# Optimization experiments

Hardware: AMD Instinct MI355X
Metric: run time of the kernel (lower is better)

## Reference

```python
import math
import jax, jax.numpy as jnp
import numpy as np

MAX_RADIUS = 10.0
N_BASIS = 10   # number_of_basis
H = 100        # radial MLP hidden width
EPS = 1e-6


def _radial(r, w1, w2, w3):
    """CosineBasisModel: cosine-bump radial basis followed by a swish MLP.
    r: [B,N,N] pair distances -> [B,N,N,C*C] per-pair kernel weights."""
    radii = jnp.linspace(0.0, MAX_RADIUS, N_BASIS)
    step = radii[1] - radii[0]
    u = (r[..., None] - radii) / step * (jnp.pi / 2)            # [B,N,N,R]
    basis = jnp.where(jnp.abs(u) < jnp.pi / 2, jnp.cos(u) ** 2, 0.0)
    h1 = jax.nn.silu(basis @ w1 * (1.0 / math.sqrt(N_BASIS)))  # swish, fan-in norm (e3nn FC)
    h2 = jax.nn.silu(h1 @ w2 * (1.0 / math.sqrt(H)))
    return h2 @ w3 * (1.0 / math.sqrt(H))                       # [B,N,N,C*C]


def setup_inputs() -> dict:
    key = jax.random.key(0)
    ks = jax.random.split(key, 10)
    B, N1, N2, C = 8, 32, 32, 64
    return {
        "input1": jax.random.normal(ks[0], (B, N1, C), jnp.float32),
        "input2": jax.random.normal(ks[1], (B, N2, C), jnp.float32),
        "xyz1": jax.random.normal(ks[2], (B, N1, 3), jnp.float32) * 3.0,
        "xyz2": jax.random.normal(ks[3], (B, N2, 3), jnp.float32) * 3.0,
        "mask": jnp.ones((B, N1 + N2), jnp.int32),
        "w1": jax.random.normal(ks[4], (N_BASIS, H), jnp.float32),
        "w2": jax.random.normal(ks[5], (H, H), jnp.float32),
        "w3": jax.random.normal(ks[6], (H, C * C), jnp.float32),
        "fc3_w": jax.random.normal(ks[7], (C, C), jnp.float32),
        "fc2_w": jax.random.normal(ks[8], (C, 1), jnp.float32),
    }


def reference(input1, input2, xyz1, xyz2, mask, w1, w2, w3, fc3_w, fc2_w):
    x = jnp.concatenate((input1, input2), axis=1)        # [B,N,C]
    xyz = jnp.concatenate((xyz1, xyz2), axis=1)          # [B,N,3]
    B, N, C = x.shape
    # continuous-filter convolution: per-pair radial kernel, all-pairs scatter-sum
    diff = xyz[:, :, None, :] - xyz[:, None, :, :]       # [B,N,N,3]
    r = jnp.sqrt(jnp.sum(diff * diff, axis=-1) + 1e-12)  # [B,N,N]
    K = _radial(r, w1, w2, w3).reshape(B, N, N, C, C)    # [B,N,N,Cout,Cin]
    x = jnp.einsum('zaboi,zbi->zao', K, x) * (1.0 / math.sqrt(N))
    # Norm over irreps: for l=0 scalar irreps the norm is |x|
    x = jnp.abs(x)
    x = jnp.where(mask[:, :, None] != 0, x, 0.0)
    x = jnp.sum(x, axis=1)                               # [B,C]
    mean = x.mean(-1, keepdims=True)
    std = jnp.std(x, axis=-1, ddof=1, keepdims=True)     # torch.std is unbiased
    x = (x - mean) / (std + EPS)
    x = jax.nn.leaky_relu(x @ fc3_w * (1.0 / math.sqrt(C)))
    x = x @ fc2_w * (1.0 / math.sqrt(C))
    return jax.nn.sigmoid(x).reshape(-1)                 # [B]
```

## Files before the change

kernel.cpp:

```cpp
#include <hip/hip_runtime.h>
#include <math.h>

#define NB 10
#define HH 100
#define TABN 2048
#define TAB_MAX 11.2f
#define INV_DELTA ((float)TABN / TAB_MAX)


__global__ __launch_bounds__(256) void tm_kernel(
    const float* __restrict__ in1, const float* __restrict__ in2,
    const float* __restrict__ w1, const float* __restrict__ w2,
    const float* __restrict__ w3,
    float* __restrict__ tab, float* __restrict__ Mout)
{
    __shared__ float s_w1[NB * HH];
    __shared__ float s_basis[8][NB];
    __shared__ float s_h1[8][HH];
    __shared__ float s_x[16][64];

    int tid = threadIdx.x;

    if (blockIdx.x < 257) {
        for (int i = tid; i < NB * HH; i += 256) s_w1[i] = w1[i];

        int p0 = blockIdx.x * 8;
        const float DELTA = TAB_MAX / (float)TABN;
        const float STEP = 10.0f / 9.0f;
        const float HALF_PI = 1.57079632679489662f;

        if (tid < 8 * NB) {
            int p = tid / NB, j = tid % NB;
            float r = (float)(p0 + p) * DELTA;
            float u = (r - (float)j * STEP) * (HALF_PI / STEP);
            float c = __cosf(u);
            s_basis[p][j] = (fabsf(u) < HALF_PI) ? c * c : 0.0f;
        }
        __syncthreads();

        const float inv_sqrt10 = 0.31622776601683794f;
        for (int task = tid; task < 8 * HH; task += 256) {
            int p = task / HH, k = task % HH;
            float acc = 0.f;
            #pragma unroll
            for (int j = 0; j < NB; ++j) acc += s_basis[p][j] * s_w1[j * HH + k];
            acc *= inv_sqrt10;
            float sg = 1.0f / (1.0f + __expf(-acc));
            s_h1[p][k] = acc * sg;
        }
        __syncthreads();

        if (tid < 8 * 25) {
            int p = tid / 25, k2g = tid % 25;
            int idx = p0 + p;
            float4 acc = make_float4(0.f, 0.f, 0.f, 0.f);
            #pragma unroll 4
            for (int k = 0; k < HH; ++k) {
                float hv = s_h1[p][k];
                float4 wv = *(const float4*)(w2 + (size_t)k * HH + k2g * 4);
                acc.x += hv * wv.x; acc.y += hv * wv.y; acc.z += hv * wv.z; acc.w += hv * wv.w;
            }
            if (idx <= TABN) {
                float4 o; float a;
                a = acc.x * 0.1f; o.x = a / (1.0f + __expf(-a));
                a = acc.y * 0.1f; o.y = a / (1.0f + __expf(-a));
                a = acc.z * 0.1f; o.z = a / (1.0f + __expf(-a));
                a = acc.w * 0.1f; o.w = a / (1.0f + __expf(-a));
                *(float4*)(tab + (size_t)idx * HH + k2g * 4) = o;
            }
        }
    } else {
        int m = blockIdx.x - 257;
        int zbg = m / 7, yc = m % 7;

        {
            int lz = tid >> 4, q = tid & 15;
            int zb = zbg * 16 + lz;
            int z = zb >> 6, b = zb & 63;
            const float* src = (b < 32) ? (in1 + (size_t)(z * 32 + b) * 64)
                                        : (in2 + (size_t)(z * 32 + (b - 32)) * 64);
            *(float4*)&s_x[lz][q * 4] = *(const float4*)(src + q * 4);
        }
        __syncthreads();

        int task = yc * 256 + tid;
        if (task < 1600) {
            int h = task >> 4, og = task & 15;
            const float* wbase = w3 + (size_t)h * 4096 + og * 4 * 64;

            float4 acc[16];
            #pragma unroll
            for (int l = 0; l < 16; ++l) acc[l] = make_float4(0.f, 0.f, 0.f, 0.f);

            const float4* sx4 = (const float4*)s_x;
            #pragma unroll 2
            for (int i4 = 0; i4 < 16; ++i4) {
                float4 wa = *(const float4*)(wbase + 0 * 64 + i4 * 4);
                float4 wb = *(const float4*)(wbase + 1 * 64 + i4 * 4);
                float4 wc = *(const float4*)(wbase + 2 * 64 + i4 * 4);
                float4 wd = *(const float4*)(wbase + 3 * 64 + i4 * 4);
                #pragma unroll
                for (int l = 0; l < 16; ++l) {
                    float4 xv = sx4[l * 16 + i4];
                    acc[l].x += wa.x * xv.x + wa.y * xv.y + wa.z * xv.z + wa.w * xv.w;
                    acc[l].y += wb.x * xv.x + wb.y * xv.y + wb.z * xv.z + wb.w * xv.w;
                    acc[l].z += wc.x * xv.x + wc.y * xv.y + wc.z * xv.z + wc.w * xv.w;
                    acc[l].w += wd.x * xv.x + wd.y * xv.y + wd.z * xv.z + wd.w * xv.w;
                }
            }
            #pragma unroll
            for (int l = 0; l < 16; ++l) {
                int zb = zbg * 16 + l;
                *(float4*)(Mout + (size_t)zb * 6400 + h * 64 + og * 4) = acc[l];
            }
        }
    }
}

__global__ __launch_bounds__(256) void kernel_Y(
    const float* __restrict__ xyz1, const float* __restrict__ xyz2,
    const float* __restrict__ tab, const float* __restrict__ M,
    float* __restrict__ partial)
{
    __shared__ float s_M[100 * 64];
    __shared__ float s_h2T[100 * 64];
    __shared__ int   s_i0[64];
    __shared__ float s_f[64];

    int z = blockIdx.x, b = blockIdx.y;
    int tid = threadIdx.x;

    if (tid < 64) {
        int a = tid;
        const float* pa = (a < 32) ? (xyz1 + (size_t)(z * 32 + a) * 3)
                                   : (xyz2 + (size_t)(z * 32 + (a - 32)) * 3);
        const float* pb = (b < 32) ? (xyz1 + (size_t)(z * 32 + b) * 3)
                                   : (xyz2 + (size_t)(z * 32 + (b - 32)) * 3);
        float dx = pa[0] - pb[0], dy = pa[1] - pb[1], dz = pa[2] - pb[2];
        float r = sqrtf(dx * dx + dy * dy + dz * dz + 1e-12f);
        float t = r * INV_DELTA;
        int i0 = (int)t;
        i0 = (i0 < TABN - 1) ? i0 : (TABN - 1);
        float f = t - (float)i0;
        s_i0[a] = i0;
        s_f[a] = (f < 1.0f) ? f : 1.0f;
    }

    {
        const float4* Msrc = (const float4*)(M + (size_t)(z * 64 + b) * 6400);
        float4* sM4 = (float4*)s_M;
        for (int i = tid; i < 1600; i += 256) sM4[i] = Msrc[i];
    }
    __syncthreads();

    for (int task = tid; task < 1600; task += 256) {
        int a4 = task / 100, c = task - a4 * 100;
        float4 hv;
        #pragma unroll
        for (int k = 0; k < 4; ++k) {
            int a = a4 * 4 + k;
            int i0 = s_i0[a];
            float f = s_f[a];
            float v0 = tab[(size_t)i0 * HH + c];
            float v1 = tab[(size_t)i0 * HH + HH + c];
            ((float*)&hv)[k] = fmaf(f, v1 - v0, v0);
        }
        *(float4*)&s_h2T[c * 64 + ((a4 ^ (c & 7)) << 2)] = hv;
    }
    __syncthreads();

    int og = tid & 15, ag = tid >> 4;
    float4 acc0 = make_float4(0.f, 0.f, 0.f, 0.f);
    float4 acc1 = make_float4(0.f, 0.f, 0.f, 0.f);
    float4 acc2 = make_float4(0.f, 0.f, 0.f, 0.f);
    float4 acc3 = make_float4(0.f, 0.f, 0.f, 0.f);

    #pragma unroll 4
    for (int c = 0; c < 100; ++c) {
        float4 mv = *(const float4*)&s_M[c * 64 + og * 4];
        float4 hv = *(const float4*)&s_h2T[c * 64 + ((ag ^ (c & 7)) << 2)];
        acc0.x += hv.x * mv.x; acc0.y += hv.x * mv.y; acc0.z += hv.x * mv.z; acc0.w += hv.x * mv.w;
        acc1.x += hv.y * mv.x; acc1.y += hv.y * mv.y; acc1.z += hv.y * mv.z; acc1.w += hv.y * mv.w;
        acc2.x += hv.z * mv.x; acc2.y += hv.z * mv.y; acc2.z += hv.z * mv.z; acc2.w += hv.z * mv.w;
        acc3.x += hv.w * mv.x; acc3.y += hv.w * mv.y; acc3.z += hv.w * mv.z; acc3.w += hv.w * mv.w;
    }

    size_t base = ((size_t)(b * 8 + z) * 64 + ag * 4) * 64 + og * 4;
    *(float4*)&partial[base]       = acc0;
    *(float4*)&partial[base + 64]  = acc1;
    *(float4*)&partial[base + 128] = acc2;
    *(float4*)&partial[base + 192] = acc3;
}

__global__ __launch_bounds__(256) void kernel_red(
    const float* __restrict__ partial, const int* __restrict__ mask,
    float* __restrict__ s2)
{
    __shared__ float sred[4][64];
    int z = blockIdx.x, ac = blockIdx.y;
    int tid = threadIdx.x;
    int o = tid & 63, ar = tid >> 6;
    int a = ac * 4 + ar;

    float val = 0.f;
    #pragma unroll 8
    for (int b = 0; b < 64; ++b)
        val += partial[((size_t)(b * 8 + z) * 64 + a) * 64 + o];

    const float scale = 0.0125f;
    float m = (mask[z * 64 + a] != 0) ? 1.0f : 0.0f;
    sred[ar][o] = fabsf(val) * scale * m;
    __syncthreads();

    if (tid < 64)
        s2[((size_t)z * 16 + ac) * 64 + o] = sred[0][o] + sred[1][o] + sred[2][o] + sred[3][o];
}

__global__ __launch_bounds__(64) void kernel_final(
    const float* __restrict__ s2, const float* __restrict__ fc3w,
    const float* __restrict__ fc2w, float* __restrict__ out)
{
    __shared__ float s_sn[64];
    int z = blockIdx.x;
    int o = threadIdx.x;

    float s = 0.f;
    #pragma unroll
    for (int ac = 0; ac < 16; ++ac)
        s += s2[((size_t)z * 16 + ac) * 64 + o];

    float tot = s;
    #pragma unroll
    for (int d = 32; d >= 1; d >>= 1) tot += __shfl_xor(tot, d, 64);
    float mean = tot * (1.0f / 64.0f);
    float dv = s - mean;
    float v2 = dv * dv;
    #pragma unroll
    for (int d = 32; d >= 1; d >>= 1) v2 += __shfl_xor(v2, d, 64);
    float var = v2 * (1.0f / 63.0f);
    float sn = dv / (sqrtf(var) + 1e-6f);

    s_sn[o] = sn;
    __syncthreads();

    float acc = 0.f;
    #pragma unroll 8
    for (int i = 0; i < 64; ++i) acc += s_sn[i] * fc3w[i * 64 + o];
    acc *= 0.125f;
    float t = (acc > 0.f) ? acc : 0.01f * acc;

    float pr = t * fc2w[o];
    #pragma unroll
    for (int d = 32; d >= 1; d >>= 1) pr += __shfl_xor(pr, d, 64);
    if (o == 0) out[z] = 1.0f / (1.0f + expf(-0.125f * pr));
}

extern "C" void kernel_launch(void* const* d_in, const int* in_sizes, int n_in,
                              void* d_out, int out_size, void* d_ws, size_t ws_size,
                              hipStream_t stream) {
    const float* in1  = (const float*)d_in[0];
    const float* in2  = (const float*)d_in[1];
    const float* xyz1 = (const float*)d_in[2];
    const float* xyz2 = (const float*)d_in[3];
    const int*   mask = (const int*)d_in[4];
    const float* w1   = (const float*)d_in[5];
    const float* w2   = (const float*)d_in[6];
    const float* w3   = (const float*)d_in[7];
    const float* fc3w = (const float*)d_in[8];
    const float* fc2w = (const float*)d_in[9];
    float* out = (float*)d_out;

    float* ws      = (float*)d_ws;
    float* tab     = ws;
    float* M       = ws + 204900;
    float* partial = ws + 3481700;
    float* s2      = ws + 5578852;

    tm_kernel<<<481, 256, 0, stream>>>(in1, in2, w1, w2, w3, tab, M);
    kernel_Y<<<dim3(8, 64), 256, 0, stream>>>(xyz1, xyz2, tab, M, partial);
    kernel_red<<<dim3(8, 16), 256, 0, stream>>>(partial, mask, s2);
    kernel_final<<<8, 64, 0, stream>>>(s2, fc3w, fc2w, out);
}
```

Measured before the change: 54.87 us.

## Fuse reduction and final MLP, halve kernel_Y threads, read x directly

Merges the reduction and final-MLP kernels into one kernel, launching one 256-thread block per batch element. Each thread now sums partials across all b with float4 loads before the normalisation and MLP. kernel_Y drops to 128 threads, each computing 8 output rows instead of 4, and the partial layout changes to z-major. The M-precompute path in tm_kernel reads x straight from global memory instead of staging it in LDS. Fewer launches and less LDS traffic come at the cost of far fewer blocks in the final reduction and more register pressure in kernel_Y.

```diff
diff --git a/kernel.cpp b/kernel.cpp
--- a/kernel.cpp
+++ b/kernel.cpp
@@ -17,7 +17,6 @@
     __shared__ float s_w1[NB * HH];
     __shared__ float s_basis[8][NB];
     __shared__ float s_h1[8][HH];
-    __shared__ float s_x[16][64];
 
     int tid = threadIdx.x;
 
@@ -73,35 +72,31 @@
         int m = blockIdx.x - 257;
         int zbg = m / 7, yc = m % 7;
 
-        {
-            int lz = tid >> 4, q = tid & 15;
-            int zb = zbg * 16 + lz;
-            int z = zb >> 6, b = zb & 63;
-            const float* src = (b < 32) ? (in1 + (size_t)(z * 32 + b) * 64)
-                                        : (in2 + (size_t)(z * 32 + (b - 32)) * 64);
-            *(float4*)&s_x[lz][q * 4] = *(const float4*)(src + q * 4);
-        }
-        __syncthreads();
-
+        const float* xp[16];
+        #pragma unroll
+        for (int l = 0; l < 16; ++l) {
+            int zb = zbg * 16 + l, z = zb >> 6, b = zb & 63;
+            xp[l] = (b < 32) ? (in1 + (size_t)(z * 32 + b) * 64)
+                             : (in2 + (size_t)(z * 32 + (b - 32)) * 64);
+        }
         int task = yc * 256 + tid;
         if (task < 1600) {
             int h = task >> 4, og = task & 15;
-            const float* wbase = w3 + (size_t)h * 4096 + og * 4 * 64;
+            const float* wbase = w3 + (size_t)h * 4096 + og * 256;
 
             float4 acc[16];
             #pragma unroll
             for (int l = 0; l < 16; ++l) acc[l] = make_float4(0.f, 0.f, 0.f, 0.f);
 
-            const float4* sx4 = (const float4*)s_x;
             #pragma unroll 2
             for (int i4 = 0; i4 < 16; ++i4) {
-                float4 wa = *(const float4*)(wbase + 0 * 64 + i4 * 4);
-                float4 wb = *(const float4*)(wbase + 1 * 64 + i4 * 4);
-                float4 wc = *(const float4*)(wbase + 2 * 64 + i4 * 4);
-                float4 wd = *(const float4*)(wbase + 3 * 64 + i4 * 4);
+                float4 wa = *(const float4*)(wbase + i4 * 4);
+                float4 wb = *(const float4*)(wbase + 64 + i4 * 4);
+                float4 wc = *(const float4*)(wbase + 128 + i4 * 4);
+                float4 wd = *(const float4*)(wbase + 192 + i4 * 4);
                 #pragma unroll
                 for (int l = 0; l < 16; ++l) {
-                    float4 xv = sx4[l * 16 + i4];
+                    float4 xv = *(const float4*)(xp[l] + i4 * 4);
                     acc[l].x += wa.x * xv.x + wa.y * xv.y + wa.z * xv.z + wa.w * xv.w;
                     acc[l].y += wb.x * xv.x + wb.y * xv.y + wb.z * xv.z + wb.w * xv.w;
                     acc[l].z += wc.x * xv.x + wc.y * xv.y + wc.z * xv.z + wc.w * xv.w;
@@ -117,18 +112,18 @@
     }
 }
 
-__global__ __launch_bounds__(256) void kernel_Y(
+__global__ __launch_bounds__(128) void kernel_Y(
     const float* __restrict__ xyz1, const float* __restrict__ xyz2,
     const float* __restrict__ tab, const float* __restrict__ M,
     float* __restrict__ partial)
 {
-    __shared__ float s_M[100 * 64];
-    __shared__ float s_h2T[100 * 64];
+    __shared__ float s_M[6400];
+    __shared__ float s_h2T[6400];
     __shared__ int   s_i0[64];
     __shared__ float s_f[64];
 
-    int z = blockIdx.x, b = blockIdx.y;
-    int tid = threadIdx.x;
+    const int b = blockIdx.x, z = blockIdx.y;
+    const int tid = threadIdx.x;
 
     if (tid < 64) {
         int a = tid;
@@ -145,114 +140,132 @@
         s_i0[a] = i0;
         s_f[a] = (f < 1.0f) ? f : 1.0f;
     }
-
     {
         const float4* Msrc = (const float4*)(M + (size_t)(z * 64 + b) * 6400);
         float4* sM4 = (float4*)s_M;
-        for (int i = tid; i < 1600; i += 256) sM4[i] = Msrc[i];
-    }
-    __syncthreads();
-
-    for (int task = tid; task < 1600; task += 256) {
-        int a4 = task / 100, c = task - a4 * 100;
-        float4 hv;
+        for (int i = tid; i < 1600; i += 128) sM4[i] = Msrc[i];
+    }
+    __syncthreads();
+
+    {
+        int a4 = tid >> 3;
+        int cg2 = tid & 7;
+        int i0a[4]; float fa[4];
         #pragma unroll
         for (int k = 0; k < 4; ++k) {
-            int a = a4 * 4 + k;
-            int i0 = s_i0[a];
-            float f = s_f[a];
-            float v0 = tab[(size_t)i0 * HH + c];
-            float v1 = tab[(size_t)i0 * HH + HH + c];
-            ((float*)&hv)[k] = fmaf(f, v1 - v0, v0);
-        }
-        *(float4*)&s_h2T[c * 64 + ((a4 ^ (c & 7)) << 2)] = hv;
-    }
-    __syncthreads();
-
-    int og = tid & 15, ag = tid >> 4;
-    float4 acc0 = make_float4(0.f, 0.f, 0.f, 0.f);
-    float4 acc1 = make_float4(0.f, 0.f, 0.f, 0.f);
-    float4 acc2 = make_float4(0.f, 0.f, 0.f, 0.f);
-    float4 acc3 = make_float4(0.f, 0.f, 0.f, 0.f);
+            i0a[k] = s_i0[a4 * 4 + k];
+            fa[k]  = s_f[a4 * 4 + k];
+        }
+        for (int c = cg2; c < 100; c += 8) {
+            float4 hv;
+            #pragma unroll
+            for (int k = 0; k < 4; ++k) {
+                const float* tp = tab + (size_t)i0a[k] * HH + c;
+                float v0 = tp[0], v1 = tp[HH];
+                ((float*)&hv)[k] = fmaf(fa[k], v1 - v0, v0);
+            }
+            *(float4*)&s_h2T[c * 64 + ((a4 ^ (c & 7)) << 2)] = hv;
+        }
+    }
+    __syncthreads();
+
+    const int og = tid & 15;
+    const int ag = tid >> 4;
+    float4 acc[8];
+    #pragma unroll
+    for (int k = 0; k < 8; ++k) acc[k] = make_float4(0.f, 0.f, 0.f, 0.f);
 
     #pragma unroll 4
     for (int c = 0; c < 100; ++c) {
+        float4 hv0 = *(const float4*)&s_h2T[c * 64 + (((2 * ag) ^ (c & 7)) << 2)];
+        float4 hv1 = *(const float4*)&s_h2T[c * 64 + (((2 * ag + 1) ^ (c & 7)) << 2)];
         float4 mv = *(const float4*)&s_M[c * 64 + og * 4];
-        float4 hv = *(const float4*)&s_h2T[c * 64 + ((ag ^ (c & 7)) << 2)];
-        acc0.x += hv.x * mv.x; acc0.y += hv.x * mv.y; acc0.z += hv.x * mv.z; acc0.w += hv.x * mv.w;
-        acc1.x += hv.y * mv.x; acc1.y += hv.y * mv.y; acc1.z += hv.y * mv.z; acc1.w += hv.y * mv.w;
-        acc2.x += hv.z * mv.x; acc2.y += hv.z * mv.y; acc2.z += hv.z * mv.z; acc2.w += hv.z * mv.w;
-        acc3.x += hv.w * mv.x; acc3.y += hv.w * mv.y; acc3.z += hv.w * mv.z; acc3.w += hv.w * mv.w;
-    }
-
-    size_t base = ((size_t)(b * 8 + z) * 64 + ag * 4) * 64 + og * 4;
-    *(float4*)&partial[base]       = acc0;
-    *(float4*)&partial[base + 64]  = acc1;
-    *(float4*)&partial[base + 128] = acc2;
-    *(float4*)&partial[base + 192] = acc3;
-}
-
-__global__ __launch_bounds__(256) void kernel_red(
+        acc[0].x += hv0.x * mv.x; acc[0].y += hv0.x * mv.y; acc[0].z += hv0.x * mv.z; acc[0].w += hv0.x * mv.w;
+        acc[1].x += hv0.y * mv.x; acc[1].y += hv0.y * mv.y; acc[1].z += hv0.y * mv.z; acc[1].w += hv0.y * mv.w;
+        acc[2].x += hv0.z * mv.x; acc[2].y += hv0.z * mv.y; acc[2].z += hv0.z * mv.z; acc[2].w += hv0.z * mv.w;
+        acc[3].x += hv0.w * mv.x; acc[3].y += hv0.w * mv.y; acc[3].z += hv0.w * mv.z; acc[3].w += hv0.w * mv.w;
+        acc[4].x += hv1.x * mv.x; acc[4].y += hv1.x * mv.y; acc[4].z += hv1.x * mv.z; acc[4].w += hv1.x * mv.w;
+        acc[5].x += hv1.y * mv.x; acc[5].y += hv1.y * mv.y; acc[5].z += hv1.y * mv.z; acc[5].w += hv1.y * mv.w;
+        acc[6].x += hv1.z * mv.x; acc[6].y += hv1.z * mv.y; acc[6].z += hv1.z * mv.z; acc[6].w += hv1.z * mv.w;
+        acc[7].x += hv1.w * mv.x; acc[7].y += hv1.w * mv.y; acc[7].z += hv1.w * mv.z; acc[7].w += hv1.w * mv.w;
+    }
+
+    size_t base = ((size_t)(z * 64 + b) * 64 + ag * 8) * 64 + og * 4;
+    #pragma unroll
+    for (int k = 0; k < 8; ++k)
+        *(float4*)&partial[base + (size_t)k * 64] = acc[k];
+}
+
+__global__ __launch_bounds__(256) void kernel_rf(
     const float* __restrict__ partial, const int* __restrict__ mask,
-    float* __restrict__ s2)
+    const float* __restrict__ fc3w, const float* __restrict__ fc2w,
+    float* __restrict__ out)
 {
-    __shared__ float sred[4][64];
-    int z = blockIdx.x, ac = blockIdx.y;
-    int tid = threadIdx.x;
-    int o = tid & 63, ar = tid >> 6;
-    int a = ac * 4 + ar;
-
-    float val = 0.f;
-    #pragma unroll 8
-    for (int b = 0; b < 64; ++b)
-        val += partial[((size_t)(b * 8 + z) * 64 + a) * 64 + o];
+    __shared__ float sred[16][64];
+    __shared__ float s_sn[64];
+
+    const int z = blockIdx.x;
+    const int tid = threadIdx.x;
+    const int og = tid & 15;
+    const int ag = tid >> 4;
+
+    float4 acc[4];
+    #pragma unroll
+    for (int k = 0; k < 4; ++k) acc[k] = make_float4(0.f, 0.f, 0.f, 0.f);
+
+    for (int b = 0; b < 64; ++b) {
+        size_t base = ((size_t)(z * 64 + b) * 64 + ag * 4) * 64 + og * 4;
+        #pragma unroll
+        for (int k = 0; k < 4; ++k) {
+            float4 v = *(const float4*)&partial[base + (size_t)k * 64];
+            acc[k].x += v.x; acc[k].y += v.y; acc[k].z += v.z; acc[k].w += v.w;
+        }
+    }
 
     const float scale = 0.0125f;
-    float m = (mask[z * 64 + a] != 0) ? 1.0f : 0.0f;
-    sred[ar][o] = fabsf(val) * scale * m;
-    __syncthreads();
-
-    if (tid < 64)
-        s2[((size_t)z * 16 + ac) * 64 + o] = sred[0][o] + sred[1][o] + sred[2][o] + sred[3][o];
-}
-
-__global__ __launch_bounds__(64) void kernel_final(
-    const float* __restrict__ s2, const float* __restrict__ fc3w,
-    const float* __restrict__ fc2w, float* __restrict__ out)
-{
-    __shared__ float s_sn[64];
-    int z = blockIdx.x;
-    int o = threadIdx.x;
-
-    float s = 0.f;
-    #pragma unroll
-    for (int ac = 0; ac < 16; ++ac)
-        s += s2[((size_t)z * 16 + ac) * 64 + o];
-
-    float tot = s;
-    #pragma unroll
-    for (int d = 32; d >= 1; d >>= 1) tot += __shfl_xor(tot, d, 64);
-    float mean = tot * (1.0f / 64.0f);
-    float dv = s - mean;
-    float v2 = dv * dv;
-    #pragma unroll
-    for (int d = 32; d >= 1; d >>= 1) v2 += __shfl_xor(v2, d, 64);
-    float var = v2 * (1.0f / 63.0f);
-    float sn = dv / (sqrtf(var) + 1e-6f);
-
-    s_sn[o] = sn;
-    __syncthreads();
-
-    float acc = 0.f;
-    #pragma unroll 8
-    for (int i = 0; i < 64; ++i) acc += s_sn[i] * fc3w[i * 64 + o];
-    acc *= 0.125f;
-    float t = (acc > 0.f) ? acc : 0.01f * acc;
-
-    float pr = t * fc2w[o];
-    #pragma unroll
-    for (int d = 32; d >= 1; d >>= 1) pr += __shfl_xor(pr, d, 64);
-    if (o == 0) out[z] = 1.0f / (1.0f + expf(-0.125f * pr));
+    float4 rs = make_float4(0.f, 0.f, 0.f, 0.f);
+    #pragma unroll
+    for (int k = 0; k < 4; ++k) {
+        float m = (mask[z * 64 + ag * 4 + k] != 0) ? scale : 0.0f;
+        rs.x += fabsf(acc[k].x) * m;
+        rs.y += fabsf(acc[k].y) * m;
+        rs.z += fabsf(acc[k].z) * m;
+        rs.w += fabsf(acc[k].w) * m;
+    }
+    *(float4*)&sred[ag][og * 4] = rs;
+    __syncthreads();
+
+    if (tid < 64) {
+        int o = tid;
+        float s = 0.f;
+        #pragma unroll
+        for (int g = 0; g < 16; ++g) s += sred[g][o];
+
+        float tot = s;
+        #pragma unroll
+        for (int d = 32; d >= 1; d >>= 1) tot += __shfl_xor(tot, d, 64);
+        float mean = tot * (1.0f / 64.0f);
+        float dv = s - mean;
+        float v2 = dv * dv;
+        #pragma unroll
+        for (int d = 32; d >= 1; d >>= 1) v2 += __shfl_xor(v2, d, 64);
+        float var = v2 * (1.0f / 63.0f);
+        s_sn[o] = dv / (sqrtf(var) + 1e-6f);
+    }
+    __syncthreads();
+
+    if (tid < 64) {
+        int o = tid;
+        float accf = 0.f;
+        #pragma unroll 8
+        for (int i = 0; i < 64; ++i) accf += s_sn[i] * fc3w[i * 64 + o];
+        accf *= 0.125f;
+        float t = (accf > 0.f) ? accf : 0.01f * accf;
+        float pr = t * fc2w[o];
+        #pragma unroll
+        for (int d = 32; d >= 1; d >>= 1) pr += __shfl_xor(pr, d, 64);
+        if (o == 0) out[z] = 1.0f / (1.0f + expf(-0.125f * pr));
+    }
 }
 
 extern "C" void kernel_launch(void* const* d_in, const int* in_sizes, int n_in,
@@ -272,12 +285,10 @@
 
     float* ws      = (float*)d_ws;
     float* tab     = ws;
-    float* M       = ws + 204900;
+    float* Mg      = ws + 204900;
     float* partial = ws + 3481700;
-    float* s2      = ws + 5578852;
-
-    tm_kernel<<<481, 256, 0, stream>>>(in1, in2, w1, w2, w3, tab, M);
-    kernel_Y<<<dim3(8, 64), 256, 0, stream>>>(xyz1, xyz2, tab, M, partial);
-    kernel_red<<<dim3(8, 16), 256, 0, stream>>>(partial, mask, s2);
-    kernel_final<<<8, 64, 0, stream>>>(s2, fc3w, fc2w, out);
-}
+
+    tm_kernel<<<481, 256, 0, stream>>>(in1, in2, w1, w2, w3, tab, Mg);
+    kernel_Y<<<dim3(64, 8), 128, 0, stream>>>(xyz1, xyz2, tab, Mg, partial);
+    kernel_rf<<<8, 256, 0, stream>>>(partial, mask, fc3w, fc2w, out);
+}
```

New measurement: 72.00 us. +31.2%, slower.
